# Performance work log

Hardware: AMD Instinct MI355X
Metric: run time of the kernel (lower is better)

The kernel has to match this reference:

```python
import jax, jax.numpy as jnp
import numpy as np

DIM = 768
NUM_HEADS = 12
N_DIV = 8
T_SHIFT = 20
T_SPAN = 11
T_CUT = T_SHIFT + 1 - T_SPAN  # 10
C = DIM // NUM_HEADS          # 64 channels per head
FOLD = C // N_DIV             # 8
BATCH = 2
FRAMES = 32
K_WIN = 4
N_TOK = 196
B_TOT = BATCH * FRAMES * K_WIN  # 256


def _entmax15_last(x):
    """Exact entmax-1.5 (Peters & Martins) along the last axis."""
    x = (x - jnp.max(x, axis=-1, keepdims=True)) * 0.5
    xs = jnp.flip(jnp.sort(x, axis=-1), axis=-1)  # descending
    d = x.shape[-1]
    rho = jnp.arange(1, d + 1, dtype=x.dtype)
    mean = jnp.cumsum(xs, axis=-1) / rho
    meansq = jnp.cumsum(xs * xs, axis=-1) / rho
    ss = rho * (meansq - mean * mean)
    delta = (1.0 - ss) / rho
    pos = delta > 0
    sq = jnp.where(pos, jnp.sqrt(jnp.where(pos, delta, 1.0)), 0.0)
    tau = mean - sq
    support = jnp.sum(tau <= xs, axis=-1, keepdims=True)
    tau_star = jnp.take_along_axis(tau, support - 1, axis=-1)
    y = jnp.clip(x - tau_star, 0.0, None)
    return y * y


def entmax15(x, axis):
    return jnp.moveaxis(_entmax15_last(jnp.moveaxis(x, axis, -1)), -1, axis)


def _shift(feat, pool_w, pool_b, win_w, win_b, forward):
    # feat: [b, t, k, h, n, c]
    b, t, k, h, n, c = feat.shape
    f = N_DIV
    cp = c // f
    # 'b t k h n (c f) -> (k n h c) (b f) t'
    g = feat.reshape(b, t, k, h, n, cp, f)
    g = jnp.transpose(g, (2, 4, 3, 5, 0, 6, 1)).reshape(k * n * h * cp, b * f, t)
    pad = (T_SHIFT, 0) if forward else (0, T_SHIFT)
    g = jnp.pad(g, ((0, 0), (0, 0), pad))
    # 'b t k h n c -> b (k n t) (h c)'
    xk = jnp.transpose(feat, (0, 2, 4, 1, 3, 5)).reshape(b, k * n * t, h * c)
    attn = xk @ pool_w + pool_b                      # [b, knt, 1]
    pooled = jnp.sum(entmax15(attn, axis=1) * xk, axis=1)  # [b, dim]
    # 'b 1 (T f) -> (b f) 1 T'
    win = (pooled @ win_w + win_b).reshape(b, T_SPAN, f)
    win = jnp.transpose(win, (0, 2, 1)).reshape(b * f, 1, T_SPAN)
    win = _entmax15_last(win)
    # depthwise conv over the (b f) channel dim, batch dim = k*n*h*cp
    out = jax.lax.conv_general_dilated(
        g, win, (1,), 'VALID',
        dimension_numbers=('NCH', 'OIH', 'NCH'),
        feature_group_count=b * f)
    tp = t + T_CUT
    # '(k n h c) (b f) t -> b t k h n c f' then mean over f
    out = out.reshape(k, n, h, cp, b, f, tp)
    out = jnp.transpose(out, (4, 6, 0, 2, 1, 3, 5)).mean(axis=-1)  # [b, tp, k, h, n, cp]
    return out[:, :-T_CUT] if forward else out[:, T_CUT:]


def _pcs(x, batch_size, frame_len, fpw, fpb, bpw, bpb, fww, fwb, bww, bwb):
    B, h, n, c = x.shape
    k = B // (batch_size * frame_len)
    feat = x.reshape(batch_size, frame_len, k, h, n, c)
    fwd = _shift(feat, fpw, fpb, fww, fwb, True)
    bwd = _shift(feat, bpw, bpb, bww, bwb, False)
    out = jnp.concatenate([fwd, bwd, feat[..., 2 * FOLD:]], axis=-1)
    return out.reshape(B, h, n, c)


def setup_inputs() -> dict:
    key = jax.random.key(0)
    ks = jax.random.split(key, 6)
    s = 0.02
    return {
        'x': jax.random.normal(ks[0], (B_TOT, NUM_HEADS, N_TOK, C), dtype=jnp.float32),
        'batch_size': BATCH,
        'frame_len': FRAMES,
        'fwd_pool_w': jax.random.normal(ks[1], (DIM, 1), dtype=jnp.float32) * s,
        'fwd_pool_b': jnp.zeros((1,), dtype=jnp.float32),
        'bwd_pool_w': jax.random.normal(ks[2], (DIM, 1), dtype=jnp.float32) * s,
        'bwd_pool_b': jnp.zeros((1,), dtype=jnp.float32),
        'fwd_win_w': jax.random.normal(ks[3], (DIM, T_SPAN * N_DIV), dtype=jnp.float32) * s,
        'fwd_win_b': jnp.zeros((T_SPAN * N_DIV,), dtype=jnp.float32),
        'bwd_win_w': jax.random.normal(ks[4], (DIM, T_SPAN * N_DIV), dtype=jnp.float32) * s,
        'bwd_win_b': jnp.zeros((T_SPAN * N_DIV,), dtype=jnp.float32),
    }


def reference(x, batch_size, frame_len, fwd_pool_w, fwd_pool_b, bwd_pool_w, bwd_pool_b,
              fwd_win_w, fwd_win_b, bwd_win_w, bwd_win_b):
    return _pcs(x, batch_size, frame_len, fwd_pool_w, fwd_pool_b, bwd_pool_w, bwd_pool_b,
                fwd_win_w, fwd_win_b, bwd_win_w, bwd_win_b)
```

## Files before the change

### kernel.cpp

```cpp
#include <hip/hip_runtime.h>

#define NH 12
#define NTOK 196
#define TT 32
#define KW 4
#define NI 25088
#define TSTRIDE 602112
#define NBLKA 256
#define NWAVESA (NBLKA * 16)

__device__ int g_counter1;
__device__ int g_flag1;

__global__ __launch_bounds__(1024) void k_attn_pool(
    const float* __restrict__ x, const float4* __restrict__ wf4,
    const float4* __restrict__ wb4,
    const float* __restrict__ fww, const float* __restrict__ fwb,
    const float* __restrict__ bww, const float* __restrict__ bwb,
    float* __restrict__ attn, float* __restrict__ winb)
{
  __shared__ float4 swf[192], swb[192];
  int tid = threadIdx.x;
  int wave = tid >> 6, lane = tid & 63;
  if (tid < 192) { swf[tid] = wf4[tid]; swb[tid] = wb4[tid]; }
  __syncthreads();

  const float4* x4 = (const float4*)x;
  int gw = blockIdx.x * 16 + wave;
  int c4 = lane & 15, nq = lane >> 4;
  for (int tsk = gw; tsk < 256 * 49; tsk += NWAVESA) {
    int B = tsk / 49, ngrp = tsk % 49;
    int n = ngrp * 4 + nq;
    float accf = 0.f, accb = 0.f;
    #pragma unroll
    for (int h = 0; h < NH; h++) {
      float4 xv = x4[((B * NH + h) * NTOK + n) * 16 + c4];
      float4 wf = swf[h * 16 + c4], wb = swb[h * 16 + c4];
      accf += xv.x * wf.x + xv.y * wf.y + xv.z * wf.z + xv.w * wf.w;
      accb += xv.x * wb.x + xv.y * wb.y + xv.z * wb.z + xv.w * wb.w;
    }
    #pragma unroll
    for (int m = 1; m < 16; m <<= 1) {
      accf += __shfl_xor(accf, m);
      accb += __shfl_xor(accb, m);
    }
    if ((lane & 15) == 0) {
      int b = B >> 7, t = (B >> 2) & 31, k = B & 3;
      int i = (k * NTOK + n) * TT + t;
      attn[b * NI + i] = accf;
      attn[(2 + b) * NI + i] = accb;
    }
  }
  __syncthreads();

  __shared__ int sticket;
  if (tid == 0)
    sticket = __hip_atomic_fetch_add(&g_counter1, 1, __ATOMIC_ACQ_REL,
                                     __HIP_MEMORY_SCOPE_AGENT);
  __syncthreads();
  int ticket = sticket;
  int rank = ticket % NBLKA;
  int target = ticket / NBLKA + 1;

  if (rank < NBLKA - 4) return;

  int p = rank - (NBLKA - 4);
  int b = p & 1;
  const float* ww = (p >> 1) ? bww : fww;
  const float* wbv = (p >> 1) ? bwb : fwb;

  if (rank == NBLKA - 1 && tid == 0)
    __hip_atomic_store(&g_flag1, target, __ATOMIC_RELEASE,
                       __HIP_MEMORY_SCOPE_AGENT);

  {
    float dummy = 0.f;
    const float4* ww4 = (const float4*)ww;
    for (int q = tid; q < 768 * 88 / 4; q += 1024) {
      float4 tv = ww4[q];
      dummy += tv.x + tv.y + tv.z + tv.w;
    }
    asm volatile("" :: "v"(dummy));
  }

  if (rank != NBLKA - 1) {
    int spins = 0;
    while (__hip_atomic_load(&g_flag1, __ATOMIC_RELAXED,
                             __HIP_MEMORY_SCOPE_AGENT) < target) {
      __builtin_amdgcn_s_sleep(2);
      if (++spins > (1 << 20)) break;
    }
    (void)__hip_atomic_load(&g_flag1, __ATOMIC_ACQUIRE,
                            __HIP_MEMORY_SCOPE_AGENT);
  }

  const float* a = attn + p * NI;
  float v[25];
  float mx = -3.0e38f;
  #pragma unroll
  for (int r = 0; r < 25; r++) {
    int i = r * 1024 + tid;
    v[r] = (i < NI) ? a[i] : -3.0e38f;
    mx = fmaxf(mx, v[r]);
  }
  __shared__ float sred1[16];
  __shared__ float sred2[16];
  __shared__ float sbc;
  int wv = tid >> 6;
  #pragma unroll
  for (int m = 1; m < 64; m <<= 1) mx = fmaxf(mx, __shfl_xor(mx, m));
  if ((tid & 63) == 0) sred1[wv] = mx;
  __syncthreads();
  if (tid == 0) {
    float m2 = sred1[0];
    for (int i2 = 1; i2 < 16; i2++) m2 = fmaxf(m2, sred1[i2]);
    sbc = m2;
  }
  __syncthreads();
  float amax = sbc;
  #pragma unroll
  for (int r = 0; r < 25; r++) v[r] = 0.5f * (v[r] - amax);

  float tau = -1.0f;
  for (int it = 0; it < 8; it++) {
    float s2 = 0.f, s1 = 0.f;
    #pragma unroll
    for (int r = 0; r < 25; r++) {
      float d = fmaxf(v[r] - tau, 0.f);
      s2 += d * d;
      s1 += d;
    }
    #pragma unroll
    for (int m = 1; m < 64; m <<= 1) {
      s2 += __shfl_xor(s2, m);
      s1 += __shfl_xor(s1, m);
    }
    if ((tid & 63) == 0) { sred2[wv] = s2; sred1[wv] = s1; }
    __syncthreads();
    if (tid == 0) {
      float S2 = 0.f, S1 = 0.f;
      for (int i2 = 0; i2 < 16; i2++) { S2 += sred2[i2]; S1 += sred1[i2]; }
      sbc = tau + (S2 - 1.f) / fmaxf(2.f * S1, 1e-12f);
    }
    __syncthreads();
    tau = sbc;
    __syncthreads();
  }

  __shared__ int scnt;
  __shared__ int sidx[8192];
  __shared__ float swgt[8192];
  if (tid == 0) scnt = 0;
  __syncthreads();
  #pragma unroll
  for (int r = 0; r < 25; r++) {
    float d = v[r] - tau;
    if (d > 0.f) {
      int slot = atomicAdd(&scnt, 1);
      if (slot < 8192) { sidx[slot] = r * 1024 + tid; swgt[slot] = d * d; }
    }
  }
  __syncthreads();
  int count = min(scnt, 8192);

  __shared__ float spool[768];
  if (tid < 768) {
    int h = tid >> 6, c = tid & 63;
    float acc = 0.f;
    for (int e = 0; e < count; e++) {
      int i = sidx[e];
      float w = swgt[e];
      int t = i & 31, r2 = i >> 5;
      int n = r2 % NTOK, k = r2 / NTOK;
      int B = (b * TT + t) * KW + k;
      acc += w * x[((B * NH + h) * NTOK + n) * 64 + c];
    }
    spool[tid] = acc;
  }
  __syncthreads();

  __shared__ float part[8][88];
  __shared__ float praw[88];
  if (tid < 704) {
    int rseg = tid / 88, col = tid % 88;
    float accw = 0.f;
    #pragma unroll 8
    for (int j = 0; j < 96; j++) {
      int r = rseg * 96 + j;
      accw += spool[r] * ww[r * 88 + col];
    }
    part[rseg][col] = accw;
  }
  __syncthreads();
  if (tid < 88) {
    float s = wbv[tid];
    #pragma unroll
    for (int g = 0; g < 8; g++) s += part[g][tid];
    praw[tid] = s;
  }
  __syncthreads();
  if (tid < 8) {
    int f = tid;
    float vv[11];
    float mmx = -3.0e38f;
    #pragma unroll
    for (int j = 0; j < 11; j++) { vv[j] = praw[j * 8 + f]; mmx = fmaxf(mmx, vv[j]); }
    #pragma unroll
    for (int j = 0; j < 11; j++) vv[j] = 0.5f * (vv[j] - mmx);
    float lo = -1.f, hi = 0.f;
    for (int it = 0; it < 30; it++) {
      float mid = 0.5f * (lo + hi), s = 0.f;
      #pragma unroll
      for (int j = 0; j < 11; j++) { float d = fmaxf(vv[j] - mid, 0.f); s += d * d; }
      if (s >= 1.f) lo = mid; else hi = mid;
    }
    float tw = 0.5f * (lo + hi);
    #pragma unroll
    for (int j = 0; j < 11; j++) {
      float d = fmaxf(vv[j] - tw, 0.f);
      winb[p * 88 + f * 11 + j] = d * d * 0.125f;
    }
  }
}

__global__ __launch_bounds__(256) void k_shift(
    const float* __restrict__ x, const float* __restrict__ win,
    float* __restrict__ out)
{
  int bkh = blockIdx.y;
  int b = bkh / 48, rem = bkh % 48;
  int k = rem / 12, h = rem % 12;
  int wave = threadIdx.x >> 6, lane = threadIdx.x & 63;
  int n = blockIdx.x * 4 + wave;
  int f = lane & 7;
  float wjf[11], wjb[11];
  #pragma unroll
  for (int j = 0; j < 11; j++) {
    wjf[j] = win[b * 88 + f * 11 + j];
    wjb[j] = win[(2 + b) * 88 + f * 11 + j];
  }
  int base = ((b * 128 + k) * NH + h) * 12544 + n * 64 + lane;
  float xr[32];
  #pragma unroll
  for (int tp = 0; tp < 32; tp++) xr[tp] = x[base + tp * TSTRIDE];

  int src = (lane & 7) << 3;
  float val[32];
  float acc[32];

  #pragma unroll
  for (int t = 0; t < 32; t++) acc[t] = 0.f;
  #pragma unroll
  for (int tp = 0; tp <= 21; tp++) {
    #pragma unroll
    for (int j = 0; j < 11; j++) {
      int to = tp + 20 - j;
      if (to >= 0 && to < 32) acc[to] += wjf[j] * xr[tp];
    }
  }
  #pragma unroll
  for (int t = 0; t < 32; t++) {
    float s = acc[t];
    s += __shfl_xor(s, 1);
    s += __shfl_xor(s, 2);
    s += __shfl_xor(s, 4);
    float sf = __shfl(s, src);
    val[t] = (lane < 8) ? sf : xr[t];
  }

  #pragma unroll
  for (int t = 0; t < 32; t++) acc[t] = 0.f;
  #pragma unroll
  for (int tp = 10; tp < 32; tp++) {
    #pragma unroll
    for (int j = 0; j < 11; j++) {
      int to = tp - 10 - j;
      if (to >= 0 && to < 32) acc[to] += wjb[j] * xr[tp];
    }
  }
  #pragma unroll
  for (int t = 0; t < 32; t++) {
    float s = acc[t];
    s += __shfl_xor(s, 1);
    s += __shfl_xor(s, 2);
    s += __shfl_xor(s, 4);
    float sb = __shfl(s, src);
    if (lane >= 8 && lane < 16) val[t] = sb;
    __builtin_nontemporal_store(val[t], &out[base + t * TSTRIDE]);
  }
}

extern "C" void kernel_launch(void* const* d_in, const int* in_sizes, int n_in,
                              void* d_out, int out_size, void* d_ws, size_t ws_size,
                              hipStream_t stream)
{
  (void)in_sizes; (void)n_in; (void)out_size; (void)ws_size;
  const float* x   = (const float*)d_in[0];
  const float* fpw = (const float*)d_in[3];
  const float* bpw = (const float*)d_in[5];
  const float* fww = (const float*)d_in[7];
  const float* fwb = (const float*)d_in[8];
  const float* bww = (const float*)d_in[9];
  const float* bwb = (const float*)d_in[10];
  float* out = (float*)d_out;

  float* W    = (float*)d_ws;
  float* attn = W;
  float* winb = attn + 4 * NI;

  k_attn_pool<<<NBLKA, 1024, 0, stream>>>(x, (const float4*)fpw,
                                          (const float4*)bpw, fww, fwb,
                                          bww, bwb, attn, winb);
  dim3 g5(49, 96);
  k_shift<<<g5, 256, 0, stream>>>(x, winb, out);
}
```

Baseline: 352.2 us.

## Parallelize sparse pooled gather across all waves and remove serial reduction barriers

Each block's pooled weighted sum over the entmax support was done by 768 threads, each looping serially over every support entry. Now the support entries are split across all 16 waves, each lane accumulates 12 heads, and the partial sums are combined through shared memory. The tau Newton iterations also drop the single-thread reduction and two extra barriers: every thread sums the double-buffered per-wave partials itself. The support buffer is halved to 4096 entries, which frees shared memory for the partial-sum array but would silently truncate a larger support.

```diff
diff --git a/kernel.cpp b/kernel.cpp
--- a/kernel.cpp
+++ b/kernel.cpp
@@ -103,26 +103,22 @@
     v[r] = (i < NI) ? a[i] : -3.0e38f;
     mx = fmaxf(mx, v[r]);
   }
-  __shared__ float sred1[16];
-  __shared__ float sred2[16];
-  __shared__ float sbc;
-  int wv = tid >> 6;
+
+  __shared__ float sM[16];
+  __shared__ float sA[2][16], sB[2][16];
   #pragma unroll
   for (int m = 1; m < 64; m <<= 1) mx = fmaxf(mx, __shfl_xor(mx, m));
-  if ((tid & 63) == 0) sred1[wv] = mx;
-  __syncthreads();
-  if (tid == 0) {
-    float m2 = sred1[0];
-    for (int i2 = 1; i2 < 16; i2++) m2 = fmaxf(m2, sred1[i2]);
-    sbc = m2;
-  }
-  __syncthreads();
-  float amax = sbc;
+  if (lane == 0) sM[wave] = mx;
+  __syncthreads();
+  float amax = sM[0];
+  #pragma unroll
+  for (int i2 = 1; i2 < 16; i2++) amax = fmaxf(amax, sM[i2]);
   #pragma unroll
   for (int r = 0; r < 25; r++) v[r] = 0.5f * (v[r] - amax);
 
   float tau = -1.0f;
   for (int it = 0; it < 8; it++) {
+    int buf = it & 1;
     float s2 = 0.f, s1 = 0.f;
     #pragma unroll
     for (int r = 0; r < 25; r++) {
@@ -135,21 +131,17 @@
       s2 += __shfl_xor(s2, m);
       s1 += __shfl_xor(s1, m);
     }
-    if ((tid & 63) == 0) { sred2[wv] = s2; sred1[wv] = s1; }
+    if (lane == 0) { sA[buf][wave] = s2; sB[buf][wave] = s1; }
     __syncthreads();
-    if (tid == 0) {
-      float S2 = 0.f, S1 = 0.f;
-      for (int i2 = 0; i2 < 16; i2++) { S2 += sred2[i2]; S1 += sred1[i2]; }
-      sbc = tau + (S2 - 1.f) / fmaxf(2.f * S1, 1e-12f);
-    }
-    __syncthreads();
-    tau = sbc;
-    __syncthreads();
+    float S2 = 0.f, S1 = 0.f;
+    #pragma unroll
+    for (int i2 = 0; i2 < 16; i2++) { S2 += sA[buf][i2]; S1 += sB[buf][i2]; }
+    tau = tau + (S2 - 1.f) / fmaxf(2.f * S1, 1e-12f);
   }
 
   __shared__ int scnt;
-  __shared__ int sidx[8192];
-  __shared__ float swgt[8192];
+  __shared__ int sidx[4096];
+  __shared__ float swgt[4096];
   if (tid == 0) scnt = 0;
   __syncthreads();
   #pragma unroll
@@ -157,25 +149,42 @@
     float d = v[r] - tau;
     if (d > 0.f) {
       int slot = atomicAdd(&scnt, 1);
-      if (slot < 8192) { sidx[slot] = r * 1024 + tid; swgt[slot] = d * d; }
-    }
-  }
-  __syncthreads();
-  int count = min(scnt, 8192);
-
+      if (slot < 4096) { sidx[slot] = r * 1024 + tid; swgt[slot] = d * d; }
+    }
+  }
+  __syncthreads();
+  int count = min(scnt, 4096);
+
+  __shared__ float spool8[8][768];
   __shared__ float spool[768];
+  float acc12[12];
+  #pragma unroll
+  for (int h = 0; h < 12; h++) acc12[h] = 0.f;
+  for (int e = wave; e < count; e += 16) {
+    int i = sidx[e];
+    float w = swgt[e];
+    int t = i & 31, r2 = i >> 5;
+    int n = r2 % NTOK, k = r2 / NTOK;
+    int B = (b * TT + t) * KW + k;
+    const float* xb = x + (size_t)B * (NH * NTOK * 64) + n * 64 + lane;
+    #pragma unroll
+    for (int h = 0; h < 12; h++) acc12[h] += w * xb[h * (NTOK * 64)];
+  }
+  if (wave >= 8) {
+    #pragma unroll
+    for (int h = 0; h < 12; h++) spool8[wave - 8][h * 64 + lane] = acc12[h];
+  }
+  __syncthreads();
+  if (wave < 8) {
+    #pragma unroll
+    for (int h = 0; h < 12; h++) spool8[wave][h * 64 + lane] += acc12[h];
+  }
+  __syncthreads();
   if (tid < 768) {
-    int h = tid >> 6, c = tid & 63;
-    float acc = 0.f;
-    for (int e = 0; e < count; e++) {
-      int i = sidx[e];
-      float w = swgt[e];
-      int t = i & 31, r2 = i >> 5;
-      int n = r2 % NTOK, k = r2 / NTOK;
-      int B = (b * TT + t) * KW + k;
-      acc += w * x[((B * NH + h) * NTOK + n) * 64 + c];
-    }
-    spool[tid] = acc;
+    float s = 0.f;
+    #pragma unroll
+    for (int g = 0; g < 8; g++) s += spool8[g][tid];
+    spool[tid] = s;
   }
   __syncthreads();
 
```

Result: no change. 350.1 us (-0.6%).
